# Kernel tuning notes

Hardware: AMD Instinct MI355X
Metric: run time of the kernel (lower is better)

## Reference

```python
import jax, jax.numpy as jnp
import numpy as np

N = 16384   # total gate nodes (64 graphs x 256 gates)
B = 64      # graphs in batch
E = 49152   # directed edges (avg in-degree 3)
Q = 32      # qubit_num
F = 256     # feat_dim
D = 2 * F   # node feature dim = 512
H = 2       # heads
A = 128     # action_num


def _gatv2(x, wl, wr, att, b, src, dst, n):
    # PyG GATv2Conv (concat=True, share_weights=False, negative_slope=0.2)
    h, c = att.shape
    xl = (x @ wl).reshape(n, h, c)   # source-side projection [N,H,C]
    xr = (x @ wr).reshape(n, h, c)   # target-side projection [N,H,C]
    e = jax.nn.leaky_relu(xl[src] + xr[dst], 0.2)       # [E,H,C]
    logit = jnp.einsum('ehc,hc->eh', e, att)             # [E,H]
    m = jax.ops.segment_max(logit, dst, num_segments=n)  # softmax over in-edges per target
    p = jnp.exp(logit - m[dst])
    den = jax.ops.segment_sum(p, dst, num_segments=n)
    alpha = p / den[dst]                                 # [E,H]
    out = jax.ops.segment_sum(alpha[:, :, None] * xl[src], dst, num_segments=n)
    return out.reshape(n, h * c) + b


def _forward(x, xt_w1, xt_b1, xt_w2, xt_b2,
             g0_wl, g0_wr, g0_att, g0_b,
             g1_wl, g1_wr, g1_att, g1_b,
             g2_wl, g2_wr, g2_att, g2_b,
             g3_wl, g3_wr, g3_att, g3_b,
             g4_wl, g4_wr, g4_att, g4_b,
             ln_w, ln_b, aggr_t,
             m_w1, m_b1, m_w2, m_b2, m_w3, m_b3,
             edge_index, batch):
    lr = lambda v: jax.nn.leaky_relu(v, 0.01)
    # x_trans: Linear -> LeakyReLU -> Linear, then fold qubit-pairs into one node
    h0 = lr(x @ xt_w1 + xt_b1) @ xt_w2 + xt_b2           # [2N, F]
    cx = h0.reshape(-1, D)                               # [N, 2F]
    n = cx.shape[0]
    # GATv2Conv default add_self_loops=True (inputs contain no self loops)
    sl = jnp.arange(n, dtype=edge_index.dtype)
    src = jnp.concatenate([edge_index[0], sl])
    dst = jnp.concatenate([edge_index[1], sl])
    res = cx
    h = lr(_gatv2(cx, g0_wl, g0_wr, g0_att, g0_b, src, dst, n))
    for wl_, wr_, att_, b_ in ((g1_wl, g1_wr, g1_att, g1_b),
                               (g2_wl, g2_wr, g2_att, g2_b),
                               (g3_wl, g3_wr, g3_att, g3_b)):
        h = lr(_gatv2(h, wl_, wr_, att_, b_, src, dst, n))
    h = lr(_gatv2(h, g4_wl, g4_wr, g4_att, g4_b, src, dst, n))
    h = h + res                                           # residual [N, 2F]
    # PyG LayerNorm(mode='graph'): normalize over nodes AND channels per graph
    cnt = jax.ops.segment_sum(jnp.ones((n,), h.dtype), batch, num_segments=B)
    norm = cnt * h.shape[1]
    mean = jax.ops.segment_sum(h.sum(-1), batch, num_segments=B) / norm
    hc = h - mean[batch][:, None]
    var = jax.ops.segment_sum((hc * hc).sum(-1), batch, num_segments=B) / norm
    h = hc / jnp.sqrt(var + 1e-5)[batch][:, None] * ln_w + ln_b
    # SoftmaxAggregation(learn=True): channel-wise softmax over nodes per graph
    logit = h * aggr_t
    mg = jax.ops.segment_max(logit, batch, num_segments=B)
    p = jnp.exp(logit - mg[batch])
    den = jax.ops.segment_sum(p, batch, num_segments=B)
    g = jax.ops.segment_sum((p / den[batch]) * h, batch, num_segments=B)  # [B, 2F]
    # head MLP 512->384->256->128
    o = lr(g @ m_w1 + m_b1)
    o = lr(o @ m_w2 + m_b2)
    return o @ m_w3 + m_b3


def setup_inputs() -> dict:
    key = jax.random.key(0)
    ks = iter(jax.random.split(key, 64))
    def rn(shp, s=0.05):
        return jax.random.normal(next(ks), shp, jnp.float32) * s
    d = {}
    d['x'] = jax.random.normal(next(ks), (2 * N, Q), jnp.float32)
    src = jax.random.randint(next(ks), (E,), 0, N, jnp.int32)
    off = jax.random.randint(next(ks), (E,), 1, N, jnp.int32)
    d['edge_index'] = jnp.stack([src, (src + off) % N])  # no self loops
    d['batch'] = jnp.arange(N, dtype=jnp.int32) // (N // B)
    d['xt_w1'] = rn((Q, F)); d['xt_b1'] = rn((F,))
    d['xt_w2'] = rn((F, F)); d['xt_b2'] = rn((F,))
    d['g0_wl'] = rn((D, H * D)); d['g0_wr'] = rn((D, H * D))
    d['g0_att'] = rn((H, D));    d['g0_b'] = rn((H * D,))
    for i in (1, 2, 3):
        d[f'g{i}_wl'] = rn((H * D, H * D)); d[f'g{i}_wr'] = rn((H * D, H * D))
        d[f'g{i}_att'] = rn((H, D));        d[f'g{i}_b'] = rn((H * D,))
    d['g4_wl'] = rn((H * D, D)); d['g4_wr'] = rn((H * D, D))
    d['g4_att'] = rn((1, D));    d['g4_b'] = rn((D,))
    d['ln_w'] = jnp.ones((D,), jnp.float32); d['ln_b'] = jnp.zeros((D,), jnp.float32)
    d['aggr_t'] = jnp.array(1.0, jnp.float32)
    d['m_w1'] = rn((D, 384)); d['m_b1'] = rn((384,))
    d['m_w2'] = rn((384, 256)); d['m_b2'] = rn((256,))
    d['m_w3'] = rn((256, A)); d['m_b3'] = rn((A,))
    return d


def reference(x, edge_index, batch, xt_w1, xt_b1, xt_w2, xt_b2,
              g0_wl, g0_wr, g0_att, g0_b,
              g1_wl, g1_wr, g1_att, g1_b,
              g2_wl, g2_wr, g2_att, g2_b,
              g3_wl, g3_wr, g3_att, g3_b,
              g4_wl, g4_wr, g4_att, g4_b,
              ln_w, ln_b, aggr_t,
              m_w1, m_b1, m_w2, m_b2, m_w3, m_b3):
    return _forward(x, xt_w1, xt_b1, xt_w2, xt_b2,
                    g0_wl, g0_wr, g0_att, g0_b,
                    g1_wl, g1_wr, g1_att, g1_b,
                    g2_wl, g2_wr, g2_att, g2_b,
                    g3_wl, g3_wr, g3_att, g3_b,
                    g4_wl, g4_wr, g4_att, g4_b,
                    ln_w, ln_b, aggr_t,
                    m_w1, m_b1, m_w2, m_b2, m_w3, m_b3,
                    edge_index, batch)
```

## Files before the change

### kernel.cpp

```cpp
#include <hip/hip_runtime.h>
#include <hip/hip_bf16.h>

typedef __hip_bfloat16 bf16;

#define NN 16384
#define BBG 64
#define EE 49152
#define ET (EE + NN)
#define DD 512
#define NG (NN / BBG)

__device__ __forceinline__ float b2f(bf16 v) { return __bfloat162float(v); }
__device__ __forceinline__ bf16 f2b(float v) { return __float2bfloat16(v); }
__device__ __forceinline__ float sb2f(short s) {
    unsigned u = ((unsigned)(unsigned short)s) << 16;
    return __builtin_bit_cast(float, u);
}
__device__ __forceinline__ short f2bs(float v) {
    bf16 b = f2b(v);
    return __builtin_bit_cast(short, b);
}
__device__ __forceinline__ int clampi(int v, int lo, int hi)
{
    return v < lo ? lo : (v > hi ? hi : v);
}

typedef __attribute__((ext_vector_type(8))) short bf16x8;
typedef __attribute__((ext_vector_type(4))) float f32x4;

#define AS1 __attribute__((address_space(1)))
#define AS3 __attribute__((address_space(3)))

__global__ __launch_bounds__(256) void gemm_mfma_bt(
    const bf16* __restrict__ A, const bf16* __restrict__ Bt,
    const float* __restrict__ bias, float* __restrict__ C,
    bf16* __restrict__ Cb, int M, int N, int K, float slope, int has_act)
{
    __shared__ bf16 As[128 * 32];
    __shared__ bf16 Bs[128 * 32];
    const int tid = threadIdx.x;
    const int w = tid >> 6;
    const int l = tid & 63;
    const int bm = blockIdx.y * 128;
    const int bn = blockIdx.x * 128;
    const int wrow = (w >> 1) * 64;
    const int wcol = (w & 1) * 64;
    const int quad = l >> 4;
    const int c16 = l & 15;

    const int lrow = l >> 2;
    const int lchunk = l & 3;
    const bf16* Ag = A + (size_t)(bm + w * 16 + lrow) * K + lchunk * 8;
    const bf16* Bg = Bt + (size_t)(bn + w * 16 + lrow) * K + lchunk * 8;
    char* AsB = (char*)As;
    char* BsB = (char*)Bs;

    f32x4 acc[4][4] = {};

    for (int k0 = 0; k0 < K; k0 += 32) {
        __builtin_amdgcn_global_load_lds((const AS1 void*)(Ag + k0),
            (AS3 void*)(AsB + w * 1024), 16, 0, 0);
        __builtin_amdgcn_global_load_lds((const AS1 void*)(Ag + (size_t)64 * K + k0),
            (AS3 void*)(AsB + 4096 + w * 1024), 16, 0, 0);
        __builtin_amdgcn_global_load_lds((const AS1 void*)(Bg + k0),
            (AS3 void*)(BsB + w * 1024), 16, 0, 0);
        __builtin_amdgcn_global_load_lds((const AS1 void*)(Bg + (size_t)64 * K + k0),
            (AS3 void*)(BsB + 4096 + w * 1024), 16, 0, 0);
        __syncthreads();

        bf16x8 a[4], b[4];
#pragma unroll
        for (int i = 0; i < 4; i++) {
            int ra = wrow + i * 16 + c16;
            a[i] = *(const bf16x8*)(AsB + ra * 64 + quad * 16);
            int rb = wcol + i * 16 + c16;
            b[i] = *(const bf16x8*)(BsB + rb * 64 + quad * 16);
        }
#pragma unroll
        for (int i = 0; i < 4; i++)
#pragma unroll
            for (int j = 0; j < 4; j++)
                acc[i][j] = __builtin_amdgcn_mfma_f32_16x16x32_bf16(
                    a[i], b[j], acc[i][j], 0, 0, 0);
        __syncthreads();
    }

#pragma unroll
    for (int i = 0; i < 4; i++) {
#pragma unroll
        for (int j = 0; j < 4; j++) {
            int col = bn + wcol + j * 16 + c16;
            float bv = bias ? bias[col] : 0.f;
#pragma unroll
            for (int r = 0; r < 4; r++) {
                int row = bm + wrow + i * 16 + quad * 4 + r;
                float v = acc[i][j][r] + bv;
                if (has_act) v = (v >= 0.f) ? v : v * slope;
                if (C)  C[(size_t)row * N + col] = v;
                if (Cb) Cb[(size_t)row * N + col] = f2b(v);
            }
        }
    }
}

template<int KK>
__global__ __launch_bounds__(512, 1) void gemm256_dual(
    const bf16* __restrict__ A, const bf16* __restrict__ Bt,
    bf16* __restrict__ X0, bf16* __restrict__ X1, int HC)
{
    constexpr int NT = KK / 64;
    __shared__ char smem[131072];
    char* const Abuf[2] = { smem,         smem + 65536 };
    char* const Bbuf[2] = { smem + 32768, smem + 98304 };
    const int tid = threadIdx.x;
    const int w = tid >> 6;
    const int l = tid & 63;
    const int wm = w >> 2;
    const int wn = w & 3;
    const int quad = l >> 4;
    const int c16 = l & 15;
    const int bm = blockIdx.y * 256;
    const int bn = blockIdx.x * 256;

    const int srow = w * 32 + (l >> 3);
    const int schunk = (l & 7) * 8;
    const bf16* AgS = A + (size_t)(bm + srow) * KK + schunk;
    const bf16* BgS = Bt + (size_t)(bn + srow) * KK + schunk;
    const int lbase = (w * 32) * 128;

    auto stage = [&](int k0, int buf) {
#pragma unroll
        for (int op = 0; op < 4; ++op)
            __builtin_amdgcn_global_load_lds(
                (const AS1 void*)(AgS + (size_t)(op * 8) * KK + k0),
                (AS3 void*)(Abuf[buf] + lbase + op * 1024), 16, 0, 0);
#pragma unroll
        for (int op = 0; op < 4; ++op)
            __builtin_amdgcn_global_load_lds(
                (const AS1 void*)(BgS + (size_t)(op * 8) * KK + k0),
                (AS3 void*)(Bbuf[buf] + lbase + op * 1024), 16, 0, 0);
    };

    f32x4 acc[8][4] = {};

    auto tile_compute = [&](int buf) {
        bf16x8 bfrag[4][2];
#pragma unroll
        for (int j = 0; j < 4; ++j)
#pragma unroll
            for (int ks = 0; ks < 2; ++ks) {
                int rb = wn * 64 + j * 16 + c16;
                bfrag[j][ks] = *(const bf16x8*)(Bbuf[buf] + rb * 128 + ks * 64 + quad * 16);
            }
#pragma unroll
        for (int ip = 0; ip < 4; ++ip) {
            bf16x8 afrag[2][2];
#pragma unroll
            for (int ii = 0; ii < 2; ++ii)
#pragma unroll
                for (int ks = 0; ks < 2; ++ks) {
                    int ra = wm * 128 + (ip * 2 + ii) * 16 + c16;
                    afrag[ii][ks] = *(const bf16x8*)(Abuf[buf] + ra * 128 + ks * 64 + quad * 16);
                }
            __builtin_amdgcn_s_setprio(1);
#pragma unroll
            for (int ii = 0; ii < 2; ++ii)
#pragma unroll
                for (int j = 0; j < 4; ++j)
#pragma unroll
                    for (int ks = 0; ks < 2; ++ks)
                        acc[ip * 2 + ii][j] = __builtin_amdgcn_mfma_f32_16x16x32_bf16(
                            afrag[ii][ks], bfrag[j][ks], acc[ip * 2 + ii][j], 0, 0, 0);
            __builtin_amdgcn_s_setprio(0);
        }
    };

    stage(0, 0);
    stage(64, 1);
    asm volatile("s_waitcnt vmcnt(8)" ::: "memory");
    __builtin_amdgcn_s_barrier();

#pragma unroll 1
    for (int tp = 0; tp < NT / 2; ++tp) {
        const int t0 = 2 * tp;
        tile_compute(0);
        __builtin_amdgcn_s_barrier();
        if (t0 + 2 < NT) {
            stage((t0 + 2) * 64, 0);
            asm volatile("s_waitcnt vmcnt(8)" ::: "memory");
        } else {
            asm volatile("s_waitcnt vmcnt(0)" ::: "memory");
        }
        __builtin_amdgcn_s_barrier();
        tile_compute(1);
        __builtin_amdgcn_s_barrier();
        if (t0 + 3 < NT) {
            stage((t0 + 3) * 64, 1);
            asm volatile("s_waitcnt vmcnt(8)" ::: "memory");
        } else {
            asm volatile("s_waitcnt vmcnt(0)" ::: "memory");
        }
        __builtin_amdgcn_s_barrier();
    }

#pragma unroll
    for (int i = 0; i < 8; ++i) {
#pragma unroll
        for (int j = 0; j < 4; ++j) {
            int col = bn + wn * 64 + j * 16 + c16;
            bf16* dst = (col < HC) ? (X0 + col) : (X1 + col - HC);
#pragma unroll
            for (int r = 0; r < 4; ++r) {
                int row = bm + wm * 128 + i * 16 + quad * 4 + r;
                dst[(size_t)row * HC] = f2b(acc[i][j][r]);
            }
        }
    }
}

__global__ __launch_bounds__(256) void gemm_f32(
    const float* __restrict__ A, const float* __restrict__ W,
    const float* __restrict__ bias, float* __restrict__ C,
    int M, int N, int K, float slope, int has_act)
{
    const int BK = 16;
    __shared__ float Asm[BK][64 + 1];
    __shared__ float Wsm[BK][64 + 1];
    int tid = threadIdx.x;
    int bm = blockIdx.y * 64;
    int bn = blockIdx.x * 64;
    int tr = tid >> 4;
    int tc = tid & 15;
    float acc[4][4] = {};

    for (int k0 = 0; k0 < K; k0 += BK) {
        {
            int col = tid & 15;
            int row = tid >> 4;
#pragma unroll
            for (int p = 0; p < 4; p++) {
                int r = row + p * 16;
                Asm[col][r] = A[(size_t)(bm + r) * K + k0 + col];
            }
        }
        {
            int wc = tid & 63;
            int wr = tid >> 6;
#pragma unroll
            for (int p = 0; p < 4; p++) {
                int r = wr + p * 4;
                Wsm[r][wc] = W[(size_t)(k0 + r) * N + bn + wc];
            }
        }
        __syncthreads();
#pragma unroll
        for (int kk = 0; kk < BK; kk++) {
            float a[4], w[4];
#pragma unroll
            for (int i = 0; i < 4; i++) a[i] = Asm[kk][tr * 4 + i];
#pragma unroll
            for (int j = 0; j < 4; j++) w[j] = Wsm[kk][tc * 4 + j];
#pragma unroll
            for (int i = 0; i < 4; i++)
#pragma unroll
                for (int j = 0; j < 4; j++)
                    acc[i][j] += a[i] * w[j];
        }
        __syncthreads();
    }
#pragma unroll
    for (int i = 0; i < 4; i++) {
        int r = bm + tr * 4 + i;
#pragma unroll
        for (int j = 0; j < 4; j++) {
            int cn = bn + tc * 4 + j;
            float v = acc[i][j];
            if (bias) v += bias[cn];
            if (has_act) v = (v >= 0.f) ? v : v * slope;
            C[(size_t)r * N + cn] = v;
        }
    }
}

__global__ __launch_bounds__(256) void transpose_f2b2(
    const float* __restrict__ in0, bf16* __restrict__ out0,
    const float* __restrict__ in1, bf16* __restrict__ out1, int R, int C)
{
    const float* in = blockIdx.z ? in1 : in0;
    bf16* out = blockIdx.z ? out1 : out0;
    __shared__ float tile[32][33];
    int c0 = blockIdx.x * 32;
    int r0 = blockIdx.y * 32;
    int tx = threadIdx.x & 31;
    int ty = threadIdx.x >> 5;
#pragma unroll
    for (int k = 0; k < 4; k++) {
        int r = ty + k * 8;
        tile[r][tx] = in[(size_t)(r0 + r) * C + c0 + tx];
    }
    __syncthreads();
#pragma unroll
    for (int k = 0; k < 4; k++) {
        int rr = ty + k * 8;
        out[(size_t)(c0 + rr) * R + r0 + tx] = f2b(tile[tx][rr]);
    }
}

__global__ void f2b_vec(const float* __restrict__ in, bf16* __restrict__ out, int n)
{
    int i = blockIdx.x * 256 + threadIdx.x;
    if (i < n) out[i] = f2b(in[i]);
}

__global__ void count_deg(const int* __restrict__ ei, int* __restrict__ deg)
{
    int e = blockIdx.x * 256 + threadIdx.x;
    if (e >= ET) return;
    int d = (e < EE) ? ei[EE + e] : (e - EE);
    d = clampi(d, 0, NN - 1);
    atomicAdd(&deg[d], 1);
}

__global__ __launch_bounds__(256) void scan_deg(const int* __restrict__ deg,
                                                int* __restrict__ rs)
{
    __shared__ int part[256];
    __shared__ int psum[257];
    int tid = threadIdx.x;
    const int per = NN / 256;
    int base = tid * per;
    int s = 0;
    for (int i = 0; i < per; i++) s += deg[base + i];
    part[tid] = s;
    __syncthreads();
    if (tid == 0) {
        int acc = 0;
        for (int i = 0; i < 256; i++) { psum[i] = acc; acc += part[i]; }
        psum[256] = acc;
    }
    __syncthreads();
    int acc = psum[tid];
    for (int i = 0; i < per; i++) { rs[base + i] = acc; acc += deg[base + i]; }
    if (tid == 0) rs[NN] = psum[256];
}

__global__ void fill_csr(const int* __restrict__ ei, const int* __restrict__ rs,
                         int* __restrict__ cur, int* __restrict__ csrc)
{
    int e = blockIdx.x * 256 + threadIdx.x;
    if (e >= ET) return;
    int s, d;
    if (e < EE) { s = ei[e]; d = ei[EE + e]; } else { s = d = e - EE; }
    s = clampi(s, 0, NN - 1);
    d = clampi(d, 0, NN - 1);
    int pos = atomicAdd(&cur[d], 1);
    int slot = clampi(rs[d] + pos, 0, ET - 1);
    csrc[slot] = s;
}

template<int NH>
__global__ __launch_bounds__(256, 4) void gat_wave6(
    const bf16* __restrict__ xl, const bf16* __restrict__ xr,
    const float* __restrict__ att, const float* __restrict__ bias,
    const int* __restrict__ rs, const int* __restrict__ csrc,
    const float* __restrict__ res, float* __restrict__ out_f,
    bf16* __restrict__ out_b, float* __restrict__ lnsums)
{
    constexpr int HC = NH * 512;
    constexpr int PF = 6;
    constexpr int NODES = (NH == 2) ? 8 : 4;
    const int tid = threadIdx.x;
    const int w = tid >> 6;
    const int lane = tid & 63;
    const int wave_id = blockIdx.x * 4 + w;

    int msrc[NODES];
    int sdeg[NODES];
#pragma unroll
    for (int it = 0; it < NODES; ++it) {
        int gw = wave_id * NODES + it;
        int n = (NH == 2) ? (gw >> 1) : gw;
        int st = rs[n];
        int deg = clampi(rs[n + 1] - st, 1, 64);
        st = clampi(st, 0, ET - 1);
        st = __builtin_amdgcn_readfirstlane(st);
        deg = __builtin_amdgcn_readfirstlane(deg);
        sdeg[it] = deg;
        msrc[it] = csrc[st + ((lane < deg) ? lane : deg - 1)];
    }

    float av0[8], av1[8];
    {
        f32x4 t0 = *(const f32x4*)(att + lane * 8);
        f32x4 t1 = *(const f32x4*)(att + lane * 8 + 4);
#pragma unroll
        for (int k = 0; k < 4; k++) { av0[k] = t0[k]; av0[4 + k] = t1[k]; }
        if (NH == 2) {
            f32x4 t2 = *(const f32x4*)(att + 512 + lane * 8);
            f32x4 t3 = *(const f32x4*)(att + 512 + lane * 8 + 4);
#pragma unroll
            for (int k = 0; k < 4; k++) { av1[k] = t2[k]; av1[4 + k] = t3[k]; }
        } else {
#pragma unroll
            for (int k = 0; k < 8; k++) av1[k] = av0[k];
        }
    }

    f32x4 rows[2][PF];
    f32x4 rpx[2];

    auto issue = [&](int it, int pb) {
        int gw = wave_id * NODES + it;
        int n = (NH == 2) ? (gw >> 1) : gw;
        int h = (NH == 2) ? (gw & 1) : 0;
        int cb = h * 512 + lane * 8;
        rpx[pb] = *(const f32x4*)(xr + (size_t)n * HC + cb);
        int dm1 = sdeg[it] - 1;
#pragma unroll
        for (int r = 0; r < PF; r++) {
            int idx = (r < dm1) ? r : dm1;
            int s = __builtin_amdgcn_readlane(msrc[it], idx);
            s = clampi(s, 0, NN - 1);
            rows[pb][r] = *(const f32x4*)(xl + (size_t)s * HC + cb);
        }
    };

    auto compute = [&](int it, int pb) {
        int gw = wave_id * NODES + it;
        int n = (NH == 2) ? (gw >> 1) : gw;
        int h = (NH == 2) ? (gw & 1) : 0;
        int cb = h * 512 + lane * 8;
        int deg = sdeg[it];

        float rv[8], av[8];
        {
            bf16x8 xb = __builtin_bit_cast(bf16x8, rpx[pb]);
#pragma unroll
            for (int k = 0; k < 8; k++) {
                rv[k] = sb2f(xb[k]);
                av[k] = h ? av1[k] : av0[k];
            }
        }

        float part[PF];
#pragma unroll
        for (int r = 0; r < PF; r++) {
            bf16x8 rb = __builtin_bit_cast(bf16x8, rows[pb][r]);
            float p0 = 0.f, p1 = 0.f, p2 = 0.f, p3 = 0.f;
#pragma unroll
            for (int k = 0; k < 8; k += 4) {
                float x0 = sb2f(rb[k + 0]);
                float x1 = sb2f(rb[k + 1]);
                float x2 = sb2f(rb[k + 2]);
                float x3 = sb2f(rb[k + 3]);
                float u0 = x0 + rv[k + 0]; u0 = (u0 >= 0.f) ? u0 : 0.2f * u0;
                float u1 = x1 + rv[k + 1]; u1 = (u1 >= 0.f) ? u1 : 0.2f * u1;
                float u2 = x2 + rv[k + 2]; u2 = (u2 >= 0.f) ? u2 : 0.2f * u2;
                float u3 = x3 + rv[k + 3]; u3 = (u3 >= 0.f) ? u3 : 0.2f * u3;
                p0 = fmaf(av[k + 0], u0, p0);
                p1 = fmaf(av[k + 1], u1, p1);
                p2 = fmaf(av[k + 2], u2, p2);
                p3 = fmaf(av[k + 3], u3, p3);
            }
            part[r] = (p0 + p1) + (p2 + p3);
        }

#pragma unroll
        for (int msk = 32; msk; msk >>= 1) {
#pragma unroll
            for (int r = 0; r < PF; r++) part[r] += __shfl_xor(part[r], msk);
        }

        float m = -1e30f;
#pragma unroll
        for (int r = 0; r < PF; r++) {
            float vr = (r < deg) ? part[r] : -1e30f;
            m = fmaxf(m, vr);
        }
        float den = 0.f;
        float pw[PF];
#pragma unroll
        for (int r = 0; r < PF; r++) {
            float e = __expf(part[r] - m);
            pw[r] = (r < deg) ? e : 0.f;
            den += pw[r];
        }

        float acc[8];
#pragma unroll
        for (int k = 0; k < 8; k++) acc[k] = 0.f;
#pragma unroll
        for (int r = 0; r < PF; r++) {
            bf16x8 rb = __builtin_bit_cast(bf16x8, rows[pb][r]);
#pragma unroll
            for (int k = 0; k < 8; k++)
                acc[k] = fmaf(pw[r], sb2f(rb[k]), acc[k]);
        }

        if (deg > PF) {
            for (int i = PF; i < deg; i++) {
                int s = __builtin_amdgcn_readlane(msrc[it], i);
                s = clampi(s, 0, NN - 1);
                f32x4 rw = *(const f32x4*)(xl + (size_t)s * HC + cb);
                bf16x8 rb = __builtin_bit_cast(bf16x8, rw);
                float pt = 0.f;
#pragma unroll
                for (int k = 0; k < 8; k++) {
                    float x = sb2f(rb[k]);
                    float u = x + rv[k];
                    u = (u >= 0.f) ? u : 0.2f * u;
                    pt = fmaf(av[k], u, pt);
                }
#pragma unroll
                for (int msk = 32; msk; msk >>= 1) pt += __shfl_xor(pt, msk);
                float mn = fmaxf(m, pt);
                float rr = __expf(m - mn);
                float pi = __expf(pt - mn);
                m = mn;
                den = den * rr + pi;
#pragma unroll
                for (int k = 0; k < 8; k++) {
                    float x = sb2f(rb[k]);
                    acc[k] = fmaf(acc[k], rr, pi * x);
                }
            }
        }

        float inv = 1.f / den;
        f32x4 b0 = *(const f32x4*)(bias + cb);
        f32x4 b1 = *(const f32x4*)(bias + cb + 4);
        float vals[8];
#pragma unroll
        for (int k = 0; k < 8; k++) {
            float bv = (k < 4) ? b0[k] : b1[k - 4];
            float v = fmaf(acc[k], inv, bv);
            v = (v >= 0.f) ? v : 0.01f * v;
            vals[k] = v;
        }
        if (res) {
            float ls = 0.f, ls2 = 0.f;
#pragma unroll
            for (int k = 0; k < 8; k++) {
                vals[k] += res[(size_t)n * HC + cb + k];
                ls += vals[k];
                ls2 += vals[k] * vals[k];
            }
#pragma unroll
            for (int v = 0; v < 2; v++) {
                f32x4 ov;
#pragma unroll
                for (int k = 0; k < 4; k++) ov[k] = vals[v * 4 + k];
                *(f32x4*)(out_f + (size_t)n * HC + cb + v * 4) = ov;
            }
            if (lnsums) {
#pragma unroll
                for (int msk = 32; msk; msk >>= 1) {
                    ls += __shfl_xor(ls, msk);
                    ls2 += __shfl_xor(ls2, msk);
                }
                if (lane == 0) {
                    int g = n >> 8;
                    atomicAdd(&lnsums[g], ls);
                    atomicAdd(&lnsums[BBG + g], ls2);
                }
            }
        } else {
            bf16x8 ov;
#pragma unroll
            for (int k = 0; k < 8; k++) ov[k] = f2bs(vals[k]);
            *(bf16x8*)(out_b + (size_t)n * HC + cb) = ov;
        }
    };

    issue(0, 0);
#pragma unroll
    for (int it = 0; it < NODES; ++it) {
        int pb = it & 1;
        if (it + 1 < NODES) issue(it + 1, pb ^ 1);
        compute(it, pb);
    }
}

template<int NH>
__global__ __launch_bounds__(256) void gat_wave7(
    const bf16* __restrict__ xl, const bf16* __restrict__ xr,
    const float* __restrict__ att, const float* __restrict__ bias,
    const int* __restrict__ rs, const int* __restrict__ csrc,
    const float* __restrict__ res, float* __restrict__ out_f,
    bf16* __restrict__ out_b, float* __restrict__ lnsums)
{
    constexpr int HC = NH * 512;
    constexpr int PF = 6;
    constexpr int NODES = (NH == 2) ? 8 : 4;
    constexpr int WPB = 4;
    constexpr int SLOTS = 7;
    __shared__ char smem[WPB * 2 * SLOTS * 1024];

    const int tid = threadIdx.x;
    const int w = tid >> 6;
    const int lane = tid & 63;
    const int wave_id = blockIdx.x * WPB + w;

    int msrc[NODES];
    int sdeg[NODES];
#pragma unroll
    for (int it = 0; it < NODES; ++it) {
        int gw = wave_id * NODES + it;
        int n = (NH == 2) ? (gw >> 1) : gw;
        int st = rs[n];
        int deg = clampi(rs[n + 1] - st, 1, 64);
        st = clampi(st, 0, ET - 1);
        st = __builtin_amdgcn_readfirstlane(st);
        deg = __builtin_amdgcn_readfirstlane(deg);
        sdeg[it] = deg;
        msrc[it] = csrc[st + ((lane < deg) ? lane : deg - 1)];
    }

    float av0[8], av1[8], bv0[8], bv1[8];
    {
        f32x4 t0 = *(const f32x4*)(att + lane * 8);
        f32x4 t1 = *(const f32x4*)(att + lane * 8 + 4);
        f32x4 u0 = *(const f32x4*)(bias + lane * 8);
        f32x4 u1 = *(const f32x4*)(bias + lane * 8 + 4);
#pragma unroll
        for (int k = 0; k < 4; k++) {
            av0[k] = t0[k]; av0[4 + k] = t1[k];
            bv0[k] = u0[k]; bv0[4 + k] = u1[k];
        }
        if (NH == 2) {
            f32x4 t2 = *(const f32x4*)(att + 512 + lane * 8);
            f32x4 t3 = *(const f32x4*)(att + 512 + lane * 8 + 4);
            f32x4 u2 = *(const f32x4*)(bias + 512 + lane * 8);
            f32x4 u3 = *(const f32x4*)(bias + 512 + lane * 8 + 4);
#pragma unroll
            for (int k = 0; k < 4; k++) {
                av1[k] = t2[k]; av1[4 + k] = t3[k];
                bv1[k] = u2[k]; bv1[4 + k] = u3[k];
            }
        } else {
#pragma unroll
            for (int k = 0; k < 8; k++) { av1[k] = av0[k]; bv1[k] = bv0[k]; }
        }
    }

    auto issue = [&](int it, int pb) {
        int gw = wave_id * NODES + it;
        int n = (NH == 2) ? (gw >> 1) : gw;
        int h = (NH == 2) ? (gw & 1) : 0;
        char* buf = smem + (size_t)((w * 2 + pb) * SLOTS) * 1024;
        const bf16* xrrow = xr + (size_t)n * HC + h * 512 + lane * 8;
        __builtin_amdgcn_global_load_lds((const AS1 void*)xrrow,
            (AS3 void*)buf, 16, 0, 0);
        int dm1 = sdeg[it] - 1;
#pragma unroll
        for (int r = 0; r < PF; r++) {
            int idx = (r < dm1) ? r : dm1;
            int s = __builtin_amdgcn_readlane(msrc[it], idx);
            s = clampi(s, 0, NN - 1);
            const bf16* row = xl + (size_t)s * HC + h * 512 + lane * 8;
            __builtin_amdgcn_global_load_lds((const AS1 void*)row,
                (AS3 void*)(buf + (1 + r) * 1024), 16, 0, 0);
        }
    };

    auto compute = [&](int it, int pb) {
        int gw = wave_id * NODES + it;
        int n = (NH == 2) ? (gw >> 1) : gw;
        int h = (NH == 2) ? (gw & 1) : 0;
        int cb = h * 512 + lane * 8;
        int deg = sdeg[it];
        char* buf = smem + (size_t)((w * 2 + pb) * SLOTS) * 1024;

        float rv[8], av[8];
        {
            bf16x8 xb = *(const bf16x8*)(buf + lane * 16);
#pragma unroll
            for (int k = 0; k < 8; k++) {
                rv[k] = sb2f(xb[k]);
                av[k] = h ? av1[k] : av0[k];
            }
        }
        bf16x8 rloc[PF];
#pragma unroll
        for (int r = 0; r < PF; r++)
            rloc[r] = *(const bf16x8*)(buf + (1 + r) * 1024 + lane * 16);

        float part[PF];
#pragma unroll
        for (int r = 0; r < PF; r++) {
            float p0 = 0.f, p1 = 0.f, p2 = 0.f, p3 = 0.f;
#pragma unroll
            for (int k = 0; k < 8; k += 4) {
                float x0 = sb2f(rloc[r][k + 0]);
                float x1 = sb2f(rloc[r][k + 1]);
                float x2 = sb2f(rloc[r][k + 2]);
                float x3 = sb2f(rloc[r][k + 3]);
                float u0 = x0 + rv[k + 0]; u0 = (u0 >= 0.f) ? u0 : 0.2f * u0;
                float u1 = x1 + rv[k + 1]; u1 = (u1 >= 0.f) ? u1 : 0.2f * u1;
                float u2 = x2 + rv[k + 2]; u2 = (u2 >= 0.f) ? u2 : 0.2f * u2;
                float u3 = x3 + rv[k + 3]; u3 = (u3 >= 0.f) ? u3 : 0.2f * u3;
                p0 = fmaf(av[k + 0], u0, p0);
                p1 = fmaf(av[k + 1], u1, p1);
                p2 = fmaf(av[k + 2], u2, p2);
                p3 = fmaf(av[k + 3], u3, p3);
            }
            part[r] = (p0 + p1) + (p2 + p3);
        }

#pragma unroll
        for (int msk = 32; msk; msk >>= 1) {
#pragma unroll
            for (int r = 0; r < PF; r++) part[r] += __shfl_xor(part[r], msk);
        }

        float m = -1e30f;
#pragma unroll
        for (int r = 0; r < PF; r++) {
            float vr = (r < deg) ? part[r] : -1e30f;
            m = fmaxf(m, vr);
        }
        float den = 0.f;
        float pw[PF];
#pragma unroll
        for (int r = 0; r < PF; r++) {
            float e = __expf(part[r] - m);
            pw[r] = (r < deg) ? e : 0.f;
            den += pw[r];
        }

        float acc[8];
#pragma unroll
        for (int k = 0; k < 8; k++) acc[k] = 0.f;
#pragma unroll
        for (int r = 0; r < PF; r++) {
#pragma unroll
            for (int k = 0; k < 8; k++)
                acc[k] = fmaf(pw[r], sb2f(rloc[r][k]), acc[k]);
        }

        if (deg > PF) {
            for (int i = PF; i < deg; i++) {
                int s = __builtin_amdgcn_readlane(msrc[it], i);
                s = clampi(s, 0, NN - 1);
                f32x4 rw = *(const f32x4*)(xl + (size_t)s * HC + cb);
                bf16x8 rb = __builtin_bit_cast(bf16x8, rw);
                float pt = 0.f;
#pragma unroll
                for (int k = 0; k < 8; k++) {
                    float x = sb2f(rb[k]);
                    float u = x + rv[k];
                    u = (u >= 0.f) ? u : 0.2f * u;
                    pt = fmaf(av[k], u, pt);
                }
#pragma unroll
                for (int msk = 32; msk; msk >>= 1) pt += __shfl_xor(pt, msk);
                float mn = fmaxf(m, pt);
                float rr = __expf(m - mn);
                float pi = __expf(pt - mn);
                m = mn;
                den = den * rr + pi;
#pragma unroll
                for (int k = 0; k < 8; k++) {
                    float x = sb2f(rb[k]);
                    acc[k] = fmaf(acc[k], rr, pi * x);
                }
            }
        }

        float inv = 1.f / den;
        float vals[8];
#pragma unroll
        for (int k = 0; k < 8; k++) {
            float bv = h ? bv1[k] : bv0[k];
            float v = fmaf(acc[k], inv, bv);
            v = (v >= 0.f) ? v : 0.01f * v;
            vals[k] = v;
        }
        bf16x8 ov;
#pragma unroll
        for (int k = 0; k < 8; k++) ov[k] = f2bs(vals[k]);
        *(bf16x8*)(out_b + (size_t)n * HC + cb) = ov;
    };

    issue(0, 0);
#pragma unroll
    for (int it = 0; it < NODES; ++it) {
        int pb = it & 1;
        if (it + 1 < NODES) {
            issue(it + 1, pb ^ 1);
            asm volatile("s_waitcnt vmcnt(7)" ::: "memory");
        } else {
            asm volatile("s_waitcnt vmcnt(0)" ::: "memory");
        }
        __builtin_amdgcn_sched_barrier(0);
        compute(it, pb);
    }
}

__global__ __launch_bounds__(256) void aggr_partial(
    const float* __restrict__ h, const float* __restrict__ lnsums,
    const float* __restrict__ lnw, const float* __restrict__ lnb,
    const float* __restrict__ t_, float* __restrict__ pm,
    float* __restrict__ pd, float* __restrict__ pa)
{
    int g = blockIdx.x, ch = blockIdx.y, nk = blockIdx.z;
    int tid = threadIdx.x;
    int c = ch * 256 + tid;
    const float tot = (float)(NG * DD);
    float S = lnsums[g], S2 = lnsums[BBG + g];
    float mu = S / tot;
    float iv = rsqrtf(fmaxf(S2 / tot - mu * mu, 0.f) + 1e-5f);
    float w = lnw[c], b = lnb[c], t = t_[0];
    size_t base = (size_t)g * NG * DD + (size_t)nk * 32 * DD + c;
    float m = -1e30f, den = 0.f, acc = 0.f;
    for (int i = 0; i < 32; i++) {
        float hn = (h[base + (size_t)i * DD] - mu) * iv * w + b;
        float lg = hn * t;
        if (lg > m) {
            float r = __expf(m - lg);
            den *= r; acc *= r; m = lg;
        }
        float p = __expf(lg - m);
        den += p; acc += p * hn;
    }
    size_t idx = (((size_t)g * 2 + ch) * 8 + nk) * 256 + tid;
    pm[idx] = m; pd[idx] = den; pa[idx] = acc;
}

__global__ __launch_bounds__(256) void aggr_combine(
    const float* __restrict__ pm, const float* __restrict__ pd,
    const float* __restrict__ pa, float* __restrict__ gout)
{
    int g = blockIdx.x, ch = blockIdx.y;
    int tid = threadIdx.x;
    size_t base = (((size_t)g * 2 + ch) * 8) * 256 + tid;
    float m = -1e30f;
#pragma unroll
    for (int k = 0; k < 8; k++) m = fmaxf(m, pm[base + k * 256]);
    float den = 0.f, acc = 0.f;
#pragma unroll
    for (int k = 0; k < 8; k++) {
        float r = __expf(pm[base + k * 256] - m);
        den += pd[base + k * 256] * r;
        acc += pa[base + k * 256] * r;
    }
    gout[(size_t)g * DD + ch * 256 + tid] = acc / den;
}

extern "C" void kernel_launch(void* const* d_in, const int* in_sizes, int n_in,
                              void* d_out, int out_size, void* d_ws, size_t ws_size,
                              hipStream_t stream)
{
    const float* x      = (const float*)d_in[0];
    const int*   ei     = (const int*)d_in[1];
    const float* xt_w1  = (const float*)d_in[3];
    const float* xt_b1  = (const float*)d_in[4];
    const float* xt_w2  = (const float*)d_in[5];
    const float* xt_b2  = (const float*)d_in[6];
    const float* ln_w   = (const float*)d_in[27];
    const float* ln_b   = (const float*)d_in[28];
    const float* aggr_t = (const float*)d_in[29];
    const float* m_w1   = (const float*)d_in[30];
    const float* m_b1   = (const float*)d_in[31];
    const float* m_w2   = (const float*)d_in[32];
    const float* m_b2   = (const float*)d_in[33];
    const float* m_w3   = (const float*)d_in[34];
    const float* m_b3   = (const float*)d_in[35];
    float* out = (float*)d_out;

    char* p = (char*)d_ws;
    auto take = [&](size_t bytes) {
        char* r = p;
        p += (bytes + 255) & ~(size_t)255;
        return r;
    };
    int* i_deg     = (int*)take((size_t)(NN + 1) * 4);
    int* i_rs      = (int*)take((size_t)(NN + 1) * 4);
    int* i_cur     = (int*)take((size_t)NN * 4);
    int* i_src     = (int*)take((size_t)ET * 4);
    float* f_sums  = (float*)take((size_t)2 * BBG * 4);
    float* f_pm    = (float*)take((size_t)BBG * 2 * 8 * 256 * 4);
    float* f_pd    = (float*)take((size_t)BBG * 2 * 8 * 256 * 4);
    float* f_pa    = (float*)take((size_t)BBG * 2 * 8 * 256 * 4);
    float* b_g     = (float*)take((size_t)BBG * DD * 4);
    float* b_m1    = (float*)take((size_t)BBG * 384 * 4);
    float* b_m2    = (float*)take((size_t)BBG * 256 * 4);
    float* b_res   = (float*)take((size_t)NN * DD * 4);
    float* b_h     = (float*)take((size_t)NN * DD * 4);
    bf16* b_resb   = (bf16*)take((size_t)NN * DD * 2);
    bf16* b_hb     = (bf16*)take((size_t)NN * 1024 * 2);
    bf16* b_xlb    = (bf16*)take((size_t)NN * 1024 * 2);
    bf16* b_xrb    = (bf16*)take((size_t)NN * 1024 * 2);
    bf16* b_xb     = (bf16*)take((size_t)2 * NN * 32 * 2);
    bf16* b_wcat   = (bf16*)take((size_t)2048 * 1024 * 2);
    bf16* b_w1b    = (bf16*)take((size_t)32 * 256 * 2);
    bf16* b_w2b    = (bf16*)take((size_t)256 * 256 * 2);
    bf16* b_t1b = b_hb;

    dim3 blk(256);

    hipMemsetAsync(i_deg, 0, (size_t)(NN + 1) * 4, stream);
    hipMemsetAsync(i_cur, 0, (size_t)NN * 4, stream);
    hipMemsetAsync(f_sums, 0, (size_t)2 * BBG * 4, stream);
    count_deg<<<ET / 256, blk, 0, stream>>>(ei, i_deg);
    scan_deg<<<1, blk, 0, stream>>>(i_deg, i_rs);
    fill_csr<<<ET / 256, blk, 0, stream>>>(ei, i_rs, i_cur, i_src);

    f2b_vec<<<(2 * NN * 32 + 255) / 256, blk, 0, stream>>>(x, b_xb, 2 * NN * 32);
    transpose_f2b2<<<dim3(256 / 32, 32 / 32, 1), blk, 0, stream>>>(
        xt_w1, b_w1b, xt_w1, b_w1b, 32, 256);
    transpose_f2b2<<<dim3(256 / 32, 256 / 32, 1), blk, 0, stream>>>(
        xt_w2, b_w2b, xt_w2, b_w2b, 256, 256);

    gemm_mfma_bt<<<dim3(256 / 128, 32768 / 128), blk, 0, stream>>>(
        b_xb, b_w1b, xt_b1, (float*)nullptr, b_t1b, 32768, 256, 32, 0.01f, 1);
    gemm_mfma_bt<<<dim3(256 / 128, 32768 / 128), blk, 0, stream>>>(
        b_t1b, b_w2b, xt_b2, b_res, b_resb, 32768, 256, 256, 0.f, 0);

    for (int L = 0; L < 5; L++) {
        const float* wl  = (const float*)d_in[7 + 4 * L];
        const float* wr  = (const float*)d_in[8 + 4 * L];
        const float* att = (const float*)d_in[9 + 4 * L];
        const float* gb  = (const float*)d_in[10 + 4 * L];
        int Fin = (L == 0) ? 512 : 1024;
        int HC  = (L == 4) ? 512 : 1024;
        const bf16* hin = (L == 0) ? b_resb : b_hb;

        transpose_f2b2<<<dim3(HC / 32, Fin / 32, 2), blk, 0, stream>>>(
            wl, b_wcat, wr, b_wcat + (size_t)HC * Fin, Fin, HC);
        if (L == 0)
            gemm256_dual<512><<<dim3(2048 / 256, NN / 256), dim3(512), 0, stream>>>(
                hin, b_wcat, b_xlb, b_xrb, 1024);
        else if (L == 4)
            gemm256_dual<1024><<<dim3(1024 / 256, NN / 256), dim3(512), 0, stream>>>(
                hin, b_wcat, b_xlb, b_xrb, 512);
        else
            gemm256_dual<1024><<<dim3(2048 / 256, NN / 256), dim3(512), 0, stream>>>(
                hin, b_wcat, b_xlb, b_xrb, 1024);

        if (L == 4) {
            gat_wave6<1><<<1024, blk, 0, stream>>>(
                b_xlb, b_xrb, att, gb, i_rs, i_src,
                b_res, b_h, (bf16*)nullptr, f_sums);
        } else {
            gat_wave7<2><<<1024, blk, 0, stream>>>(
                b_xlb, b_xrb, att, gb, i_rs, i_src,
                (const float*)nullptr, (float*)nullptr, b_hb, (float*)nullptr);
        }
    }

    aggr_partial<<<dim3(BBG, 2, 8), blk, 0, stream>>>(
        b_h, f_sums, ln_w, ln_b, aggr_t, f_pm, f_pd, f_pa);
    aggr_combine<<<dim3(BBG, 2), blk, 0, stream>>>(f_pm, f_pd, f_pa, b_g);

    gemm_f32<<<dim3(384 / 64, 1), blk, 0, stream>>>(
        b_g, m_w1, m_b1, b_m1, 64, 384, 512, 0.01f, 1);
    gemm_f32<<<dim3(256 / 64, 1), blk, 0, stream>>>(
        b_m1, m_w2, m_b2, b_m2, 64, 256, 384, 0.01f, 1);
    gemm_f32<<<dim3(128 / 64, 1), blk, 0, stream>>>(
        b_m2, m_w3, m_b3, out, 64, 128, 256, 0.f, 0);
}
```

Before: 1.021 ms.

## Restructure GAT projection GEMM into 8-phase half-K pipelined schedule

Replaces the two-buffer full-tile GEMM loop with an 8-phase schedule. Each K tile is split into two 32-wide halves, and each phase computes half of the wave's rows. Global-to-LDS loads for upcoming half-tiles are issued in the middle of compute phases, with finer waitcnt/barrier points, so memory traffic overlaps with MFMA work. Launch bounds change to allow 2 blocks per CU, though the 128KB shared buffer likely still limits occupancy to one block. The extra barriers per tile add synchronization overhead.

```diff
diff --git a/kernel.cpp b/kernel.cpp
--- a/kernel.cpp
+++ b/kernel.cpp
@@ -104,14 +104,12 @@
 }
 
 template<int KK>
-__global__ __launch_bounds__(512, 1) void gemm256_dual(
+__global__ __launch_bounds__(512, 2) void gemm256_8ph(
     const bf16* __restrict__ A, const bf16* __restrict__ Bt,
     bf16* __restrict__ X0, bf16* __restrict__ X1, int HC)
 {
     constexpr int NT = KK / 64;
     __shared__ char smem[131072];
-    char* const Abuf[2] = { smem,         smem + 65536 };
-    char* const Bbuf[2] = { smem + 32768, smem + 98304 };
     const int tid = threadIdx.x;
     const int w = tid >> 6;
     const int l = tid & 63;
@@ -122,86 +120,81 @@
     const int bm = blockIdx.y * 256;
     const int bn = blockIdx.x * 256;
 
-    const int srow = w * 32 + (l >> 3);
-    const int schunk = (l & 7) * 8;
-    const bf16* AgS = A + (size_t)(bm + srow) * KK + schunk;
-    const bf16* BgS = Bt + (size_t)(bn + srow) * KK + schunk;
-    const int lbase = (w * 32) * 128;
-
-    auto stage = [&](int k0, int buf) {
-#pragma unroll
-        for (int op = 0; op < 4; ++op)
+    const int r_loc = l >> 2;
+    const int qc = l & 3;
+    const int srow = w * 32;
+    const bf16* Ag = A + (size_t)(bm + srow + r_loc) * KK + qc * 8;
+    const bf16* Bg = Bt + (size_t)(bn + srow + r_loc) * KK + qc * 8;
+
+    auto stage = [&](int t, int kh, int db) {
+        const int koff = t * 64 + kh * 32;
+        char* ab = smem + (db * 2 + kh) * 16384 + srow * 64;
+        char* bb = ab + 65536;
+#pragma unroll
+        for (int win = 0; win < 2; ++win)
             __builtin_amdgcn_global_load_lds(
-                (const AS1 void*)(AgS + (size_t)(op * 8) * KK + k0),
-                (AS3 void*)(Abuf[buf] + lbase + op * 1024), 16, 0, 0);
-#pragma unroll
-        for (int op = 0; op < 4; ++op)
+                (const AS1 void*)(Ag + (size_t)(win * 16) * KK + koff),
+                (AS3 void*)(ab + win * 1024), 16, 0, 0);
+#pragma unroll
+        for (int win = 0; win < 2; ++win)
             __builtin_amdgcn_global_load_lds(
-                (const AS1 void*)(BgS + (size_t)(op * 8) * KK + k0),
-                (AS3 void*)(Bbuf[buf] + lbase + op * 1024), 16, 0, 0);
+                (const AS1 void*)(Bg + (size_t)(win * 16) * KK + koff),
+                (AS3 void*)(bb + win * 1024), 16, 0, 0);
     };
 
     f32x4 acc[8][4] = {};
 
-    auto tile_compute = [&](int buf) {
-        bf16x8 bfrag[4][2];
-#pragma unroll
-        for (int j = 0; j < 4; ++j)
-#pragma unroll
-            for (int ks = 0; ks < 2; ++ks) {
-                int rb = wn * 64 + j * 16 + c16;
-                bfrag[j][ks] = *(const bf16x8*)(Bbuf[buf] + rb * 128 + ks * 64 + quad * 16);
-            }
-#pragma unroll
-        for (int ip = 0; ip < 4; ++ip) {
-            bf16x8 afrag[2][2];
-#pragma unroll
-            for (int ii = 0; ii < 2; ++ii)
-#pragma unroll
-                for (int ks = 0; ks < 2; ++ks) {
-                    int ra = wm * 128 + (ip * 2 + ii) * 16 + c16;
-                    afrag[ii][ks] = *(const bf16x8*)(Abuf[buf] + ra * 128 + ks * 64 + quad * 16);
-                }
-            __builtin_amdgcn_s_setprio(1);
-#pragma unroll
-            for (int ii = 0; ii < 2; ++ii)
-#pragma unroll
-                for (int j = 0; j < 4; ++j)
-#pragma unroll
-                    for (int ks = 0; ks < 2; ++ks)
-                        acc[ip * 2 + ii][j] = __builtin_amdgcn_mfma_f32_16x16x32_bf16(
-                            afrag[ii][ks], bfrag[j][ks], acc[ip * 2 + ii][j], 0, 0, 0);
-            __builtin_amdgcn_s_setprio(0);
-        }
+    auto phase = [&](int db, int rh, int kh,
+                     int st_t, int st_kh, int st_db, bool do_stage, bool do_vm) {
+        const char* Ab = smem + (db * 2 + kh) * 16384;
+        const char* Bb = Ab + 65536;
+        bf16x8 af[4], bfr[4];
+#pragma unroll
+        for (int rt = 0; rt < 4; ++rt) {
+            int row = wm * 128 + rh * 64 + rt * 16 + c16;
+            af[rt] = *(const bf16x8*)(Ab + row * 64 + quad * 16);
+        }
+#pragma unroll
+        for (int ct = 0; ct < 4; ++ct) {
+            int row = wn * 64 + ct * 16 + c16;
+            bfr[ct] = *(const bf16x8*)(Bb + row * 64 + quad * 16);
+        }
+        if (do_stage) stage(st_t, st_kh, st_db);
+        __builtin_amdgcn_s_setprio(1);
+#pragma unroll
+        for (int rt = 0; rt < 4; ++rt)
+#pragma unroll
+            for (int ct = 0; ct < 4; ++ct)
+                acc[rh * 4 + rt][ct] = __builtin_amdgcn_mfma_f32_16x16x32_bf16(
+                    af[rt], bfr[ct], acc[rh * 4 + rt][ct], 0, 0, 0);
+        __builtin_amdgcn_s_setprio(0);
+        if (do_vm) asm volatile("s_waitcnt vmcnt(8) lgkmcnt(0)" ::: "memory");
+        else       asm volatile("s_waitcnt lgkmcnt(0)" ::: "memory");
+        __builtin_amdgcn_sched_barrier(0);
+        __builtin_amdgcn_s_barrier();
     };
 
-    stage(0, 0);
-    stage(64, 1);
+    stage(0, 0, 0);
+    stage(0, 1, 0);
+    stage(1, 0, 1);
     asm volatile("s_waitcnt vmcnt(8)" ::: "memory");
     __builtin_amdgcn_s_barrier();
 
 #pragma unroll 1
-    for (int tp = 0; tp < NT / 2; ++tp) {
-        const int t0 = 2 * tp;
-        tile_compute(0);
-        __builtin_amdgcn_s_barrier();
-        if (t0 + 2 < NT) {
-            stage((t0 + 2) * 64, 0);
-            asm volatile("s_waitcnt vmcnt(8)" ::: "memory");
-        } else {
-            asm volatile("s_waitcnt vmcnt(0)" ::: "memory");
-        }
-        __builtin_amdgcn_s_barrier();
-        tile_compute(1);
-        __builtin_amdgcn_s_barrier();
-        if (t0 + 3 < NT) {
-            stage((t0 + 3) * 64, 1);
-            asm volatile("s_waitcnt vmcnt(8)" ::: "memory");
-        } else {
-            asm volatile("s_waitcnt vmcnt(0)" ::: "memory");
-        }
-        __builtin_amdgcn_s_barrier();
-    }
+    for (int it8 = 0; it8 < NT / 2; ++it8) {
+        int s1 = 2 * it8 + 1;
+        int s2 = 2 * it8 + 2; if (s2 > NT - 1) s2 = NT - 1;
+        int s3 = 2 * it8 + 3; if (s3 > NT - 1) s3 = NT - 1;
+        phase(0, 0, 0, s1, 1, 1, true,  false);
+        phase(0, 1, 0, 0, 0, 0, false, true);
+        phase(0, 0, 1, s2, 0, 0, true,  false);
+        phase(0, 1, 1, 0, 0, 0, false, true);
+        phase(1, 0, 0, s2, 1, 0, true,  false);
+        phase(1, 1, 0, 0, 0, 0, false, true);
+        phase(1, 0, 1, s3, 0, 1, true,  false);
+        phase(1, 1, 1, 0, 0, 0, false, true);
+    }
+    asm volatile("s_waitcnt vmcnt(0)" ::: "memory");
 
 #pragma unroll
     for (int i = 0; i < 8; ++i) {
@@ -929,13 +922,13 @@
         transpose_f2b2<<<dim3(HC / 32, Fin / 32, 2), blk, 0, stream>>>(
             wl, b_wcat, wr, b_wcat + (size_t)HC * Fin, Fin, HC);
         if (L == 0)
-            gemm256_dual<512><<<dim3(2048 / 256, NN / 256), dim3(512), 0, stream>>>(
+            gemm256_8ph<512><<<dim3(2048 / 256, NN / 256), dim3(512), 0, stream>>>(
                 hin, b_wcat, b_xlb, b_xrb, 1024);
         else if (L == 4)
-            gemm256_dual<1024><<<dim3(1024 / 256, NN / 256), dim3(512), 0, stream>>>(
+            gemm256_8ph<1024><<<dim3(1024 / 256, NN / 256), dim3(512), 0, stream>>>(
                 hin, b_wcat, b_xlb, b_xrb, 512);
         else
-            gemm256_dual<1024><<<dim3(2048 / 256, NN / 256), dim3(512), 0, stream>>>(
+            gemm256_8ph<1024><<<dim3(2048 / 256, NN / 256), dim3(512), 0, stream>>>(
                 hin, b_wcat, b_xlb, b_xrb, 1024);
 
         if (L == 4) {
```

After: 956.8 us. -6.3%, faster.
